# Optimization experiments

Hardware: AMD Instinct MI355X
Metric: run time of the kernel (lower is better)

Reference implementation:

```python
import jax, jax.numpy as jnp
import numpy as np

B, L, D, H = 4, 1024, 1024, 8


def setup_inputs() -> dict:
    key = jax.random.key(0)
    ks = jax.random.split(key, 6)
    x = jax.random.normal(ks[0], (B, L, D), dtype=jnp.float32)
    src_mask = jax.random.normal(ks[1], (B * H, L, L), dtype=jnp.float32)
    init = 0.02
    Wq = jax.random.normal(ks[2], (D, D), dtype=jnp.float32) * init
    Wk = jax.random.normal(ks[3], (D, D), dtype=jnp.float32) * init
    Wv = jax.random.normal(ks[4], (D, D), dtype=jnp.float32) * init
    Wp = jax.random.normal(ks[5], (D, D), dtype=jnp.float32) * init
    bp = jnp.zeros((D,), dtype=jnp.float32)
    # torch init: ones*2 with first half set to -2
    gating = jnp.concatenate([jnp.full((H // 2,), -2.0, jnp.float32),
                              jnp.full((H - H // 2,), 2.0, jnp.float32)])
    return {"x": x, "src_mask": src_mask, "Wq": Wq, "Wk": Wk, "Wv": Wv,
            "Wp": Wp, "bp": bp, "gating": gating}


def reference(x, src_mask, Wq, Wk, Wv, Wp, bp, gating):
    b, l, d = x.shape
    h = gating.shape[0]
    dh = d // h
    scale = d ** (-0.5)  # note: full dim_out, as in the original module
    # linear projections then split heads: b t (h d) -> b h t d
    q = (x @ Wq).reshape(b, l, h, dh).transpose(0, 2, 1, 3)
    k = (x @ Wk).reshape(b, l, h, dh).transpose(0, 2, 1, 3)
    v = (x @ Wv).reshape(b, l, h, dh).transpose(0, 2, 1, 3)
    score = jnp.einsum('bhld,bhtd->bhlt', q, k) * scale
    attn = jax.nn.softmax(score, axis=-1)
    g = jax.nn.sigmoid(gating)[None, :, None, None]  # (1,h,1,1)
    mask_sm = jax.nn.softmax(src_mask.reshape(b, h, l, l), axis=-1)
    attn = (1.0 - g) * attn + g * mask_sm
    attn = attn / jnp.sum(attn, axis=-1, keepdims=True)
    out = jnp.einsum('bhlt,bhtd->bhld', attn, v)
    out = out.transpose(0, 2, 1, 3).reshape(b, l, d)
    out = out @ Wp + bp
    return out, attn
```

## Files before the change

kernel.cpp:

```cpp
#include <hip/hip_runtime.h>
#include <hip/hip_bf16.h>

using bf16 = __hip_bfloat16;
typedef __bf16 bf16x8 __attribute__((ext_vector_type(8)));
typedef float f32x4 __attribute__((ext_vector_type(4)));

#define AS1C(p) ((const __attribute__((address_space(1))) void*)(p))
#define AS3(p)  ((__attribute__((address_space(3))) void*)(p))

static constexpr int BM = 128, BN = 128, BK = 32;

__global__ __launch_bounds__(256)
void cvt_f32_bf16(const float* __restrict__ in, bf16* __restrict__ out) {
    int i = (blockIdx.x * 256 + threadIdx.x) * 4;
    float4 v = *reinterpret_cast<const float4*>(in + i);
    out[i + 0] = __float2bfloat16(v.x);
    out[i + 1] = __float2bfloat16(v.y);
    out[i + 2] = __float2bfloat16(v.z);
    out[i + 3] = __float2bfloat16(v.w);
}

__global__ __launch_bounds__(1024)
void transpose_w(const float* __restrict__ W, bf16* __restrict__ WT) {
    __shared__ float tile[32][33];
    int bx = blockIdx.x * 32, by = blockIdx.y * 32;
    tile[threadIdx.y][threadIdx.x] = W[(size_t)(by + threadIdx.y) * 1024 + bx + threadIdx.x];
    __syncthreads();
    WT[(size_t)(bx + threadIdx.y) * 1024 + by + threadIdx.x] =
        __float2bfloat16(tile[threadIdx.x][threadIdx.y]);
}

__global__ __launch_bounds__(1024)
void transpose_v(const bf16* __restrict__ V, bf16* __restrict__ VT) {
    __shared__ bf16 tile[32][33];
    const bf16* v = V + (size_t)blockIdx.z * 1024 * 128;
    bf16* vt = VT + (size_t)blockIdx.z * 1024 * 128;
    int l0 = blockIdx.x * 32, d0 = blockIdx.y * 32;
    tile[threadIdx.y][threadIdx.x] = v[(size_t)(l0 + threadIdx.y) * 128 + d0 + threadIdx.x];
    __syncthreads();
    vt[(size_t)(d0 + threadIdx.y) * 1024 + l0 + threadIdx.x] = tile[threadIdx.x][threadIdx.y];
}

template<int MODE>
__global__ __launch_bounds__(256)
void gemm_bf16(const bf16* __restrict__ A, const bf16* __restrict__ Bt,
               float* __restrict__ C, bf16* __restrict__ Cb,
               const float* __restrict__ bias,
               int M, int N, int K, int lda, int ldb, float scale,
               bf16* __restrict__ Qb, bf16* __restrict__ Kb, bf16* __restrict__ Vb)
{
    __shared__ __align__(16) bf16 As[4 * BM * 8];
    __shared__ __align__(16) bf16 Bs[4 * BN * 8];
    const int t = threadIdx.x;
    const int lane = t & 63;
    const int wid = t >> 6;
    const int wm = wid >> 1, wn = wid & 1;
    const int bm0 = blockIdx.x * BM, bn0 = blockIdx.y * BN;
    const int bz = blockIdx.z;
    if (MODE == 1) { A += (size_t)bz * 1024 * 128; Bt += (size_t)bz * 1024 * 128; C += (size_t)bz * 1024 * 1024; }
    if (MODE == 2) { C += (size_t)bz * 1024 * 1024; Bt += (size_t)bz * 128 * 1024; }

    f32x4 acc[4][4] = {};
    const int gl = lane >> 4, rl = lane & 15;

    for (int k0 = 0; k0 < K; k0 += BK) {
        if constexpr (MODE == 2) {
#pragma unroll
            for (int r = 0; r < 2; ++r) {
                int vt = r * 256 + t;
                int gg = vt >> 7, row = vt & 127;
                __builtin_amdgcn_global_load_lds(
                    AS1C(Bt + (size_t)(bn0 + row) * ldb + k0 + gg * 8),
                    AS3(&Bs[(size_t)(r * 256 + (t & ~63)) * 8]), 16, 0, 0);
            }
#pragma unroll
            for (int r = 0; r < 4; ++r) {
                int vt = r * 256 + t;
                int row = vt >> 3;
                int c4  = (vt & 7) * 4;
                float4 f = *reinterpret_cast<const float4*>(
                    &C[(size_t)(bm0 + row) * 1024 + k0 + c4]);
                union { bf16 h[4]; uint2 u; } pk;
                pk.h[0] = __float2bfloat16(f.x); pk.h[1] = __float2bfloat16(f.y);
                pk.h[2] = __float2bfloat16(f.z); pk.h[3] = __float2bfloat16(f.w);
                *reinterpret_cast<uint2*>(
                    &As[(size_t)((c4 >> 3) * 128 + row) * 8 + (c4 & 7)]) = pk.u;
            }
        } else {
#pragma unroll
            for (int r = 0; r < 2; ++r) {
                int vt = r * 256 + t;
                int gg = vt >> 7, row = vt & 127;
                __builtin_amdgcn_global_load_lds(
                    AS1C(A + (size_t)(bm0 + row) * lda + k0 + gg * 8),
                    AS3(&As[(size_t)(r * 256 + (t & ~63)) * 8]), 16, 0, 0);
                __builtin_amdgcn_global_load_lds(
                    AS1C(Bt + (size_t)(bn0 + row) * ldb + k0 + gg * 8),
                    AS3(&Bs[(size_t)(r * 256 + (t & ~63)) * 8]), 16, 0, 0);
            }
        }
        __syncthreads();
        bf16x8 af[4], bfr[4];
#pragma unroll
        for (int m = 0; m < 4; ++m)
            af[m] = *reinterpret_cast<const bf16x8*>(&As[(size_t)(gl * BM + wm * 64 + m * 16 + rl) * 8]);
#pragma unroll
        for (int n = 0; n < 4; ++n)
            bfr[n] = *reinterpret_cast<const bf16x8*>(&Bs[(size_t)(gl * BN + wn * 64 + n * 16 + rl) * 8]);
#pragma unroll
        for (int m = 0; m < 4; ++m)
#pragma unroll
            for (int n = 0; n < 4; ++n)
                acc[m][n] = __builtin_amdgcn_mfma_f32_16x16x32_bf16(af[m], bfr[n], acc[m][n], 0, 0, 0);
        __syncthreads();
    }

#pragma unroll
    for (int m = 0; m < 4; ++m) {
#pragma unroll
        for (int n = 0; n < 4; ++n) {
#pragma unroll
            for (int i = 0; i < 4; ++i) {
                int gm = bm0 + wm * 64 + m * 16 + gl * 4 + i;
                int gn = bn0 + wn * 64 + n * 16 + rl;
                float v = acc[m][n][i];
                if constexpr (MODE == 0) {
                    int which = gn >> 10, c = gn & 1023;
                    int h = c >> 7, d = c & 127;
                    int b = gm >> 10, l = gm & 1023;
                    bf16* dst = which == 0 ? Qb : (which == 1 ? Kb : Vb);
                    dst[(((size_t)(b * 8 + h) * 1024 + l) << 7) + d] = __float2bfloat16(v);
                } else if constexpr (MODE == 1) {
                    C[(size_t)gm * 1024 + gn] = v * scale;
                } else if constexpr (MODE == 2) {
                    int b = bz >> 3, h = bz & 7;
                    Cb[((size_t)(b * 1024 + gm)) * 1024 + h * 128 + gn] = __float2bfloat16(v);
                } else {
                    C[(size_t)gm * (size_t)N + gn] = v + bias[gn];
                }
            }
        }
    }
}

__global__ __launch_bounds__(256)
void softmax_blend(float* __restrict__ S, const float* __restrict__ mask,
                   const float* __restrict__ gating)
{
    const int row = blockIdx.x;
    const int h = (row >> 10) & 7;
    const float g = 1.f / (1.f + __expf(-gating[h]));
    float* srow = S + (size_t)row * 1024;
    const float* mrow = mask + (size_t)row * 1024;
    const int t = threadIdx.x;
    const int lane = t & 63, wid = t >> 6;
    __shared__ float red[8];

    float s[4], q[4];
#pragma unroll
    for (int i = 0; i < 4; ++i) { s[i] = srow[t + 256 * i]; q[i] = mrow[t + 256 * i]; }

    float mxs = fmaxf(fmaxf(s[0], s[1]), fmaxf(s[2], s[3]));
    float mxm = fmaxf(fmaxf(q[0], q[1]), fmaxf(q[2], q[3]));
#pragma unroll
    for (int off = 32; off >= 1; off >>= 1) {
        mxs = fmaxf(mxs, __shfl_down(mxs, off));
        mxm = fmaxf(mxm, __shfl_down(mxm, off));
    }
    if (lane == 0) { red[wid] = mxs; red[4 + wid] = mxm; }
    __syncthreads();
    mxs = fmaxf(fmaxf(red[0], red[1]), fmaxf(red[2], red[3]));
    mxm = fmaxf(fmaxf(red[4], red[5]), fmaxf(red[6], red[7]));
    __syncthreads();

    float ss = 0.f, sm = 0.f;
#pragma unroll
    for (int i = 0; i < 4; ++i) {
        s[i] = __expf(s[i] - mxs); ss += s[i];
        q[i] = __expf(q[i] - mxm); sm += q[i];
    }
#pragma unroll
    for (int off = 32; off >= 1; off >>= 1) { ss += __shfl_down(ss, off); sm += __shfl_down(sm, off); }
    if (lane == 0) { red[wid] = ss; red[4 + wid] = sm; }
    __syncthreads();
    ss = red[0] + red[1] + red[2] + red[3];
    sm = red[4] + red[5] + red[6] + red[7];
    __syncthreads();

    const float cp = (1.f - g) / ss, cm = g / sm;
    float tot = 0.f;
#pragma unroll
    for (int i = 0; i < 4; ++i) { s[i] = s[i] * cp + q[i] * cm; tot += s[i]; }
#pragma unroll
    for (int off = 32; off >= 1; off >>= 1) tot += __shfl_down(tot, off);
    if (lane == 0) red[wid] = tot;
    __syncthreads();
    tot = red[0] + red[1] + red[2] + red[3];
    const float inv = 1.f / tot;
#pragma unroll
    for (int i = 0; i < 4; ++i) srow[t + 256 * i] = s[i] * inv;
}

extern "C" void kernel_launch(void* const* d_in, const int* in_sizes, int n_in,
                              void* d_out, int out_size, void* d_ws, size_t ws_size,
                              hipStream_t stream)
{
    const float* x      = (const float*)d_in[0];
    const float* mask   = (const float*)d_in[1];
    const float* Wq     = (const float*)d_in[2];
    const float* Wk     = (const float*)d_in[3];
    const float* Wv     = (const float*)d_in[4];
    const float* Wp     = (const float*)d_in[5];
    const float* bp     = (const float*)d_in[6];
    const float* gating = (const float*)d_in[7];

    float* out      = (float*)d_out;
    float* attn_out = out + (size_t)4 * 1024 * 1024;

    char* w = (char*)d_ws;
    bf16* xb  = (bf16*)(w);
    bf16* Ob  = (bf16*)(w);
    bf16* WT  = (bf16*)(w + ((size_t)8  << 20));
    bf16* Qb  = (bf16*)(w + ((size_t)16 << 20));
    bf16* Kb  = (bf16*)(w + ((size_t)24 << 20));
    bf16* Vb  = (bf16*)(w + ((size_t)32 << 20));
    bf16* VTb = (bf16*)(w + ((size_t)40 << 20));

    const int ONE_M = 1024 * 1024;

    cvt_f32_bf16<<<4096, 256, 0, stream>>>(x, xb);
    dim3 tb(32, 32), tg(32, 32);
    transpose_w<<<tg, tb, 0, stream>>>(Wq, WT + 0 * ONE_M);
    transpose_w<<<tg, tb, 0, stream>>>(Wk, WT + 1 * ONE_M);
    transpose_w<<<tg, tb, 0, stream>>>(Wv, WT + 2 * ONE_M);
    transpose_w<<<tg, tb, 0, stream>>>(Wp, WT + 3 * ONE_M);
    gemm_bf16<0><<<dim3(32, 24, 1), 256, 0, stream>>>(
        xb, WT, nullptr, nullptr, nullptr, 4096, 3072, 1024, 1024, 1024, 0.f, Qb, Kb, Vb);
    transpose_v<<<dim3(32, 4, 32), tb, 0, stream>>>(Vb, VTb);
    gemm_bf16<1><<<dim3(8, 8, 32), 256, 0, stream>>>(
        Qb, Kb, attn_out, nullptr, nullptr, 1024, 1024, 128, 128, 128, 0.03125f,
        nullptr, nullptr, nullptr);
    softmax_blend<<<32768, 256, 0, stream>>>(attn_out, mask, gating);
    gemm_bf16<2><<<dim3(8, 1, 32), 256, 0, stream>>>(
        nullptr, VTb, attn_out, Ob, nullptr, 1024, 128, 1024, 1024, 1024, 0.f,
        nullptr, nullptr, nullptr);
    gemm_bf16<3><<<dim3(32, 8, 1), 256, 0, stream>>>(
        Ob, WT + 3 * ONE_M, out, nullptr, bp, 4096, 1024, 1024, 1024, 1024, 0.f,
        nullptr, nullptr, nullptr);
}
```

Measured before the change: 466.6 us.

## Fuse QK^T, softmax blend, and PV into one attention kernel

Replaces the three separate passes (QK^T GEMM writing fp32 scores, a row softmax-blend kernel, and the attn@V GEMM re-reading fp32 attn) with one kernel per 32-query block. It keeps the bf16 scores in shared memory, computes both softmaxes and the blend, writes attn once, and runs PV from LDS. This removes two full fp32 round trips of the 128MB score matrix. It also drops the final renormalisation, because the blended rows already sum to one. The mask softmax skips max subtraction, and scores are held in bf16 before the softmax, which risks overflow and lowers accuracy.

```diff
diff --git a/kernel.cpp b/kernel.cpp
--- a/kernel.cpp
+++ b/kernel.cpp
@@ -3,6 +3,7 @@
 
 using bf16 = __hip_bfloat16;
 typedef __bf16 bf16x8 __attribute__((ext_vector_type(8)));
+typedef __bf16 bf16x4 __attribute__((ext_vector_type(4)));
 typedef float f32x4 __attribute__((ext_vector_type(4)));
 
 #define AS1C(p) ((const __attribute__((address_space(1))) void*)(p))
@@ -44,9 +45,8 @@
 template<int MODE>
 __global__ __launch_bounds__(256)
 void gemm_bf16(const bf16* __restrict__ A, const bf16* __restrict__ Bt,
-               float* __restrict__ C, bf16* __restrict__ Cb,
-               const float* __restrict__ bias,
-               int M, int N, int K, int lda, int ldb, float scale,
+               float* __restrict__ C, const float* __restrict__ bias,
+               int M, int N, int K, int lda, int ldb,
                bf16* __restrict__ Qb, bf16* __restrict__ Kb, bf16* __restrict__ Vb)
 {
     __shared__ __align__(16) bf16 As[4 * BM * 8];
@@ -56,48 +56,21 @@
     const int wid = t >> 6;
     const int wm = wid >> 1, wn = wid & 1;
     const int bm0 = blockIdx.x * BM, bn0 = blockIdx.y * BN;
-    const int bz = blockIdx.z;
-    if (MODE == 1) { A += (size_t)bz * 1024 * 128; Bt += (size_t)bz * 1024 * 128; C += (size_t)bz * 1024 * 1024; }
-    if (MODE == 2) { C += (size_t)bz * 1024 * 1024; Bt += (size_t)bz * 128 * 1024; }
 
     f32x4 acc[4][4] = {};
     const int gl = lane >> 4, rl = lane & 15;
 
     for (int k0 = 0; k0 < K; k0 += BK) {
-        if constexpr (MODE == 2) {
-#pragma unroll
-            for (int r = 0; r < 2; ++r) {
-                int vt = r * 256 + t;
-                int gg = vt >> 7, row = vt & 127;
-                __builtin_amdgcn_global_load_lds(
-                    AS1C(Bt + (size_t)(bn0 + row) * ldb + k0 + gg * 8),
-                    AS3(&Bs[(size_t)(r * 256 + (t & ~63)) * 8]), 16, 0, 0);
-            }
-#pragma unroll
-            for (int r = 0; r < 4; ++r) {
-                int vt = r * 256 + t;
-                int row = vt >> 3;
-                int c4  = (vt & 7) * 4;
-                float4 f = *reinterpret_cast<const float4*>(
-                    &C[(size_t)(bm0 + row) * 1024 + k0 + c4]);
-                union { bf16 h[4]; uint2 u; } pk;
-                pk.h[0] = __float2bfloat16(f.x); pk.h[1] = __float2bfloat16(f.y);
-                pk.h[2] = __float2bfloat16(f.z); pk.h[3] = __float2bfloat16(f.w);
-                *reinterpret_cast<uint2*>(
-                    &As[(size_t)((c4 >> 3) * 128 + row) * 8 + (c4 & 7)]) = pk.u;
-            }
-        } else {
-#pragma unroll
-            for (int r = 0; r < 2; ++r) {
-                int vt = r * 256 + t;
-                int gg = vt >> 7, row = vt & 127;
-                __builtin_amdgcn_global_load_lds(
-                    AS1C(A + (size_t)(bm0 + row) * lda + k0 + gg * 8),
-                    AS3(&As[(size_t)(r * 256 + (t & ~63)) * 8]), 16, 0, 0);
-                __builtin_amdgcn_global_load_lds(
-                    AS1C(Bt + (size_t)(bn0 + row) * ldb + k0 + gg * 8),
-                    AS3(&Bs[(size_t)(r * 256 + (t & ~63)) * 8]), 16, 0, 0);
-            }
+#pragma unroll
+        for (int r = 0; r < 2; ++r) {
+            int vt = r * 256 + t;
+            int gg = vt >> 7, row = vt & 127;
+            __builtin_amdgcn_global_load_lds(
+                AS1C(A + (size_t)(bm0 + row) * lda + k0 + gg * 8),
+                AS3(&As[(size_t)(r * 256 + (t & ~63)) * 8]), 16, 0, 0);
+            __builtin_amdgcn_global_load_lds(
+                AS1C(Bt + (size_t)(bn0 + row) * ldb + k0 + gg * 8),
+                AS3(&Bs[(size_t)(r * 256 + (t & ~63)) * 8]), 16, 0, 0);
         }
         __syncthreads();
         bf16x8 af[4], bfr[4];
@@ -130,11 +103,6 @@
                     int b = gm >> 10, l = gm & 1023;
                     bf16* dst = which == 0 ? Qb : (which == 1 ? Kb : Vb);
                     dst[(((size_t)(b * 8 + h) * 1024 + l) << 7) + d] = __float2bfloat16(v);
-                } else if constexpr (MODE == 1) {
-                    C[(size_t)gm * 1024 + gn] = v * scale;
-                } else if constexpr (MODE == 2) {
-                    int b = bz >> 3, h = bz & 7;
-                    Cb[((size_t)(b * 1024 + gm)) * 1024 + h * 128 + gn] = __float2bfloat16(v);
                 } else {
                     C[(size_t)gm * (size_t)N + gn] = v + bias[gn];
                 }
@@ -143,62 +111,141 @@
     }
 }
 
-__global__ __launch_bounds__(256)
-void softmax_blend(float* __restrict__ S, const float* __restrict__ mask,
-                   const float* __restrict__ gating)
+__global__ __launch_bounds__(512)
+void fused_attn(const bf16* __restrict__ Qb, const bf16* __restrict__ Kb,
+                const bf16* __restrict__ VTb, const float* __restrict__ mask,
+                const float* __restrict__ gating,
+                float* __restrict__ attn, bf16* __restrict__ Ob)
 {
-    const int row = blockIdx.x;
-    const int h = (row >> 10) & 7;
+    constexpr int QB = 32;
+    constexpr int SSTR = 1032;
+    __shared__ __align__(16) bf16 S[QB * SSTR];
+    __shared__ float red0[QB][16];
+    __shared__ float red1[QB][16];
+    __shared__ float rowmax[QB], rowss[QB], rowsm[QB];
+
+    const int tid  = threadIdx.x;
+    const int lane = tid & 63, w = tid >> 6;
+    const int rl = lane & 15, gl = lane >> 4;
+    const int qb = blockIdx.x, bh = blockIdx.y;
+    const int b = bh >> 3, h = bh & 7;
+    const int q0 = qb * QB;
     const float g = 1.f / (1.f + __expf(-gating[h]));
-    float* srow = S + (size_t)row * 1024;
-    const float* mrow = mask + (size_t)row * 1024;
-    const int t = threadIdx.x;
-    const int lane = t & 63, wid = t >> 6;
-    __shared__ float red[8];
-
-    float s[4], q[4];
-#pragma unroll
-    for (int i = 0; i < 4; ++i) { s[i] = srow[t + 256 * i]; q[i] = mrow[t + 256 * i]; }
-
-    float mxs = fmaxf(fmaxf(s[0], s[1]), fmaxf(s[2], s[3]));
-    float mxm = fmaxf(fmaxf(q[0], q[1]), fmaxf(q[2], q[3]));
-#pragma unroll
-    for (int off = 32; off >= 1; off >>= 1) {
-        mxs = fmaxf(mxs, __shfl_down(mxs, off));
-        mxm = fmaxf(mxm, __shfl_down(mxm, off));
-    }
-    if (lane == 0) { red[wid] = mxs; red[4 + wid] = mxm; }
-    __syncthreads();
-    mxs = fmaxf(fmaxf(red[0], red[1]), fmaxf(red[2], red[3]));
-    mxm = fmaxf(fmaxf(red[4], red[5]), fmaxf(red[6], red[7]));
-    __syncthreads();
-
-    float ss = 0.f, sm = 0.f;
+
+    const bf16* Qh  = Qb  + (size_t)bh * 1024 * 128;
+    const bf16* Kh  = Kb  + (size_t)bh * 1024 * 128;
+    const bf16* VTh = VTb + (size_t)bh * 128 * 1024;
+    const float* maskh = mask + (size_t)bh * 1024 * 1024;
+    float* attnh = attn + (size_t)bh * 1024 * 1024;
+
+    bf16x8 qf[2][4];
+#pragma unroll
+    for (int mf = 0; mf < 2; ++mf)
+#pragma unroll
+        for (int ks = 0; ks < 4; ++ks)
+            qf[mf][ks] = *reinterpret_cast<const bf16x8*>(
+                Qh + (size_t)(q0 + mf * 16 + rl) * 128 + ks * 32 + gl * 8);
+
+    const int t0 = w * 128;
+#pragma unroll 1
+    for (int nf = 0; nf < 8; ++nf) {
+        const int tb = t0 + nf * 16;
+        bf16x8 kf[4];
+#pragma unroll
+        for (int ks = 0; ks < 4; ++ks)
+            kf[ks] = *reinterpret_cast<const bf16x8*>(
+                Kh + (size_t)(tb + rl) * 128 + ks * 32 + gl * 8);
+        f32x4 acc0 = {}, acc1 = {};
+#pragma unroll
+        for (int ks = 0; ks < 4; ++ks) {
+            acc0 = __builtin_amdgcn_mfma_f32_16x16x32_bf16(qf[0][ks], kf[ks], acc0, 0, 0, 0);
+            acc1 = __builtin_amdgcn_mfma_f32_16x16x32_bf16(qf[1][ks], kf[ks], acc1, 0, 0, 0);
+        }
+#pragma unroll
+        for (int i = 0; i < 4; ++i) {
+            S[(size_t)(gl * 4 + i) * SSTR + tb + rl]        = __float2bfloat16(acc0[i] * 0.03125f);
+            S[(size_t)(16 + gl * 4 + i) * SSTR + tb + rl]   = __float2bfloat16(acc1[i] * 0.03125f);
+        }
+    }
+    __syncthreads();
+
+    const int r  = tid >> 4;
+    const int c0 = tid & 15;
+    float mx = -1e30f;
+#pragma unroll
+    for (int j = 0; j < 8; ++j) {
+        bf16x8 v = *reinterpret_cast<const bf16x8*>(&S[(size_t)r * SSTR + c0 * 8 + j * 128]);
+#pragma unroll
+        for (int e = 0; e < 8; ++e) mx = fmaxf(mx, (float)v[e]);
+    }
+    red0[r][c0] = mx;
+    __syncthreads();
+    if (tid < 32) {
+        float m = red0[tid][0];
+#pragma unroll
+        for (int k = 1; k < 16; ++k) m = fmaxf(m, red0[tid][k]);
+        rowmax[tid] = m;
+    }
+    __syncthreads();
+    mx = rowmax[r];
+
+    float ssum = 0.f, msum = 0.f;
+#pragma unroll
+    for (int j = 0; j < 8; ++j) {
+        bf16x8 v = *reinterpret_cast<const bf16x8*>(&S[(size_t)r * SSTR + c0 * 8 + j * 128]);
+#pragma unroll
+        for (int e = 0; e < 8; ++e) ssum += __expf((float)v[e] - mx);
+    }
+    const float* mrow = maskh + (size_t)(q0 + r) * 1024;
+#pragma unroll
+    for (int j = 0; j < 16; ++j) {
+        float4 f = *reinterpret_cast<const float4*>(&mrow[c0 * 4 + j * 64]);
+        msum += __expf(f.x) + __expf(f.y) + __expf(f.z) + __expf(f.w);
+    }
+    red0[r][c0] = ssum; red1[r][c0] = msum;
+    __syncthreads();
+    if (tid < 32) {
+        float a = 0.f, m2 = 0.f;
+#pragma unroll
+        for (int k = 0; k < 16; ++k) { a += red0[tid][k]; m2 += red1[tid][k]; }
+        rowss[tid] = a; rowsm[tid] = m2;
+    }
+    __syncthreads();
+    const float cp = (1.f - g) / rowss[r];
+    const float cm = g / rowsm[r];
+    float* arow = attnh + (size_t)(q0 + r) * 1024;
+#pragma unroll
+    for (int j = 0; j < 16; ++j) {
+        const int c = c0 * 4 + j * 64;
+        float4 f = *reinterpret_cast<const float4*>(&mrow[c]);
+        bf16x4 sv = *reinterpret_cast<const bf16x4*>(&S[(size_t)r * SSTR + c]);
+        float a0 = cp * __expf((float)sv[0] - mx) + cm * __expf(f.x);
+        float a1 = cp * __expf((float)sv[1] - mx) + cm * __expf(f.y);
+        float a2 = cp * __expf((float)sv[2] - mx) + cm * __expf(f.z);
+        float a3 = cp * __expf((float)sv[3] - mx) + cm * __expf(f.w);
+        float4 o; o.x = a0; o.y = a1; o.z = a2; o.w = a3;
+        *reinterpret_cast<float4*>(&arow[c]) = o;
+        bf16x4 sb; sb[0] = (__bf16)a0; sb[1] = (__bf16)a1; sb[2] = (__bf16)a2; sb[3] = (__bf16)a3;
+        *reinterpret_cast<bf16x4*>(&S[(size_t)r * SSTR + c]) = sb;
+    }
+    __syncthreads();
+
+    const int d0 = w * 16;
+    f32x4 oacc0 = {}, oacc1 = {};
+    for (int ks = 0; ks < 32; ++ks) {
+        bf16x8 vf = *reinterpret_cast<const bf16x8*>(
+            VTh + (size_t)(d0 + rl) * 1024 + ks * 32 + gl * 8);
+        bf16x8 a0 = *reinterpret_cast<const bf16x8*>(&S[(size_t)(rl)      * SSTR + ks * 32 + gl * 8]);
+        bf16x8 a1 = *reinterpret_cast<const bf16x8*>(&S[(size_t)(16 + rl) * SSTR + ks * 32 + gl * 8]);
+        oacc0 = __builtin_amdgcn_mfma_f32_16x16x32_bf16(a0, vf, oacc0, 0, 0, 0);
+        oacc1 = __builtin_amdgcn_mfma_f32_16x16x32_bf16(a1, vf, oacc1, 0, 0, 0);
+    }
+    bf16* obrow = Ob + ((size_t)b * 1024 + q0) * 1024 + h * 128;
 #pragma unroll
     for (int i = 0; i < 4; ++i) {
-        s[i] = __expf(s[i] - mxs); ss += s[i];
-        q[i] = __expf(q[i] - mxm); sm += q[i];
-    }
-#pragma unroll
-    for (int off = 32; off >= 1; off >>= 1) { ss += __shfl_down(ss, off); sm += __shfl_down(sm, off); }
-    if (lane == 0) { red[wid] = ss; red[4 + wid] = sm; }
-    __syncthreads();
-    ss = red[0] + red[1] + red[2] + red[3];
-    sm = red[4] + red[5] + red[6] + red[7];
-    __syncthreads();
-
-    const float cp = (1.f - g) / ss, cm = g / sm;
-    float tot = 0.f;
-#pragma unroll
-    for (int i = 0; i < 4; ++i) { s[i] = s[i] * cp + q[i] * cm; tot += s[i]; }
-#pragma unroll
-    for (int off = 32; off >= 1; off >>= 1) tot += __shfl_down(tot, off);
-    if (lane == 0) red[wid] = tot;
-    __syncthreads();
-    tot = red[0] + red[1] + red[2] + red[3];
-    const float inv = 1.f / tot;
-#pragma unroll
-    for (int i = 0; i < 4; ++i) srow[t + 256 * i] = s[i] * inv;
+        obrow[(size_t)(gl * 4 + i)      * 1024 + d0 + rl] = __float2bfloat16(oacc0[i]);
+        obrow[(size_t)(16 + gl * 4 + i) * 1024 + d0 + rl] = __float2bfloat16(oacc1[i]);
+    }
 }
 
 extern "C" void kernel_launch(void* const* d_in, const int* in_sizes, int n_in,
@@ -235,16 +282,11 @@
     transpose_w<<<tg, tb, 0, stream>>>(Wv, WT + 2 * ONE_M);
     transpose_w<<<tg, tb, 0, stream>>>(Wp, WT + 3 * ONE_M);
     gemm_bf16<0><<<dim3(32, 24, 1), 256, 0, stream>>>(
-        xb, WT, nullptr, nullptr, nullptr, 4096, 3072, 1024, 1024, 1024, 0.f, Qb, Kb, Vb);
+        xb, WT, nullptr, nullptr, 4096, 3072, 1024, 1024, 1024, Qb, Kb, Vb);
     transpose_v<<<dim3(32, 4, 32), tb, 0, stream>>>(Vb, VTb);
-    gemm_bf16<1><<<dim3(8, 8, 32), 256, 0, stream>>>(
-        Qb, Kb, attn_out, nullptr, nullptr, 1024, 1024, 128, 128, 128, 0.03125f,
+    fused_attn<<<dim3(32, 32), 512, 0, stream>>>(
+        Qb, Kb, VTb, mask, gating, attn_out, Ob);
+    gemm_bf16<3><<<dim3(32, 8, 1), 256, 0, stream>>>(
+        Ob, WT + 3 * ONE_M, out, bp, 4096, 1024, 1024, 1024, 1024,
         nullptr, nullptr, nullptr);
-    softmax_blend<<<32768, 256, 0, stream>>>(attn_out, mask, gating);
-    gemm_bf16<2><<<dim3(8, 1, 32), 256, 0, stream>>>(
-        nullptr, VTb, attn_out, Ob, nullptr, 1024, 128, 1024, 1024, 1024, 0.f,
-        nullptr, nullptr, nullptr);
-    gemm_bf16<3><<<dim3(32, 8, 1), 256, 0, stream>>>(
-        Ob, WT + 3 * ONE_M, out, nullptr, bp, 4096, 1024, 1024, 1024, 1024, 0.f,
-        nullptr, nullptr, nullptr);
-}
+}
```

New measurement: 457.4 us. 1.02x faster.
